# Kernel optimization log

Hardware: AMD Instinct MI355X
Metric: run time of the kernel (lower is better)

Reference implementation:

```python
import jax, jax.numpy as jnp
import numpy as np

BETA = 6.0
LOG_2PI = float(np.log(2.0 * np.pi))


def setup_inputs() -> dict:
    key = jax.random.key(0)
    k1, k2, k3, k4 = jax.random.split(key, 4)
    B, L = 2048, 64
    kl = jax.random.uniform(k1, (B, L), dtype=jnp.float32)
    z_mean = jax.random.normal(k2, (B, L), dtype=jnp.float32)
    z_logvar = jax.random.normal(k3, (B, L), dtype=jnp.float32)
    z_sampled = jax.random.normal(k4, (B, L), dtype=jnp.float32)
    return {"kl": kl, "z_mean": z_mean, "z_logvar": z_logvar, "z_sampled": z_sampled}


def gaussian_log_density(samples, mean, log_var):
    # samples: [B,1,L], mean/log_var: [1,B,L] -> [B,B,L]
    tmp = samples - mean
    return -0.5 * (tmp * tmp * jnp.exp(-log_var) + log_var + LOG_2PI)


def total_correlation(z, z_mean, z_logvar):
    # [B, B, L]: log q(z_i_l | x_j)
    log_qz_prob = gaussian_log_density(z[:, None, :], z_mean[None, :, :], z_logvar[None, :, :])
    # sum_l logsumexp_j -> [B]
    log_qz_product = jnp.sum(jax.scipy.special.logsumexp(log_qz_prob, axis=1), axis=1)
    # logsumexp_j sum_l -> [B]
    log_qz = jax.scipy.special.logsumexp(jnp.sum(log_qz_prob, axis=2), axis=1)
    return jnp.mean(log_qz - log_qz_product)


def reference(kl, z_mean, z_logvar, z_sampled):
    kl_loss = jnp.sum(kl)
    tc = (BETA - 1.0) * total_correlation(z_sampled, z_mean, z_logvar)
    return tc + kl_loss
```

## Files before the change

kernel.cpp:

```cpp
#include <hip/hip_runtime.h>
#include <math.h>


#define NB 2048
#define NL 64
#define NE (NB * NL)
#define BVAL 12.0f

__device__ __forceinline__ float wredsum(float v) {
#pragma unroll
  for (int o = 32; o; o >>= 1) v += __shfl_xor(v, o, 64);
  return v;
}
__device__ __forceinline__ float wredmax(float v) {
#pragma unroll
  for (int o = 32; o; o >>= 1) v = fmaxf(v, __shfl_xor(v, o, 64));
  return v;
}

__global__ __launch_bounds__(256) void ka_pre(const float* __restrict__ kl,
                                              const float* __restrict__ zm,
                                              const float* __restrict__ zlv,
                                              float4* __restrict__ PK2,
                                              float* __restrict__ A2T,
                                              float* __restrict__ MA2T,
                                              float* __restrict__ QC2,
                                              float* __restrict__ KLP,
                                              float* __restrict__ Sacc,
                                              int* __restrict__ CNT) {
  const float INVLN2 = 1.4426950408889634f;
  const float LOG2PI = 1.8378770664093453f;
  int tid = threadIdx.x;
  int e = blockIdx.x * 256 + tid;
  int j = e >> 6, l = e & 63;
  float lv = zlv[e], m = zm[e];
  float a2 = -0.5f * INVLN2 * __expf(-lv);
  float b2 = -0.5f * INVLN2 * (lv + LOG2PI);
  float c1 = -2.0f * a2 * m;
  float c0 = fmaf(a2 * m, m, b2);
  PK2[e] = make_float4(a2, c1, c0 - BVAL, 0.0f);
  A2T[l * NB + j] = a2;
  MA2T[l * NB + j] = c1;
  Sacc[e] = 0.0f;
  float q = wredsum(c0);
  if (l == 0) QC2[j] = q;
  float ks = wredsum(kl[e]);
  __shared__ float sk[4];
  if (l == 0) sk[tid >> 6] = ks;
  __syncthreads();
  if (tid == 0) KLP[blockIdx.x] = sk[0] + sk[1] + sk[2] + sk[3];
  if (blockIdx.x == 0 && tid == 0) *CNT = 0;
}

__global__ __launch_bounds__(256, 8) void kb_main(const float* __restrict__ zs,
                                                  const float* __restrict__ A2T,
                                                  const float* __restrict__ MA2T,
                                                  const float* __restrict__ QC2,
                                                  const float4* __restrict__ PK2,
                                                  float* __restrict__ TPM,
                                                  float* __restrict__ TPS,
                                                  float* __restrict__ Sacc) {
  int bid = blockIdx.x;
  int jc = bid & 7;
  int i0 = (bid >> 3) * 8;
  int tid = threadIdx.x;
  int w = tid >> 6, l = tid & 63;

  __shared__ float zsh[64][8];
  if (tid < 128) {
    int k = tid >> 1, r0 = (tid & 1) * 4;
#pragma unroll
    for (int r = 0; r < 4; ++r) zsh[k][r0 + r] = zs[(i0 + r0 + r) * NL + k];
  }
  __syncthreads();
  int j = jc * 256 + tid;
  float accv[8];
  float q = QC2[j];
#pragma unroll
  for (int r = 0; r < 8; ++r) accv[r] = q;
  for (int k = 0; k < 64; ++k) {
    float av = A2T[k * NB + j];
    float mv = MA2T[k * NB + j];
    const float4* z4 = (const float4*)&zsh[k][0];
    float4 za = z4[0], zb = z4[1];
    float zk[8] = {za.x, za.y, za.z, za.w, zb.x, zb.y, zb.z, zb.w};
#pragma unroll
    for (int r = 0; r < 8; ++r) {
      accv[r] = fmaf(zk[r] * zk[r], av, accv[r]);
      accv[r] = fmaf(zk[r], mv, accv[r]);
    }
  }
  __shared__ float lm[4][8], ls[4][8];
#pragma unroll
  for (int r = 0; r < 8; ++r) {
    float mx = wredmax(accv[r]);
    if (l == 0) lm[w][r] = mx;
  }
  __syncthreads();
  float Mt[8];
#pragma unroll
  for (int r = 0; r < 8; ++r)
    Mt[r] = fmaxf(fmaxf(lm[0][r], lm[1][r]), fmaxf(lm[2][r], lm[3][r]));
#pragma unroll
  for (int r = 0; r < 8; ++r) {
    float ss = wredsum(__builtin_amdgcn_exp2f(accv[r] - Mt[r]));
    if (l == 0) ls[w][r] = ss;
  }
  __syncthreads();
  if (tid == 0) {
#pragma unroll
    for (int r = 0; r < 8; ++r) {
      TPM[(i0 + r) * 8 + jc] = Mt[r];
      TPS[(i0 + r) * 8 + jc] = ls[0][r] + ls[1][r] + ls[2][r] + ls[3][r];
    }
  }

  const float4* p = PK2 + (size_t)(jc * 256 + w * 64) * NL + l;
  float zr[8];
#pragma unroll
  for (int r = 0; r < 8; ++r) zr[r] = zs[(i0 + r) * NL + l];
  float S[8];
#pragma unroll
  for (int r = 0; r < 8; ++r) S[r] = 0.0f;
#pragma unroll 4
  for (int jj = 0; jj < 64; ++jj) {
    float4 c = p[(size_t)jj * NL];
#pragma unroll
    for (int r = 0; r < 8; ++r) {
      float lp2 = fmaf(fmaf(zr[r], c.x, c.y), zr[r], c.z);
      S[r] += __builtin_amdgcn_exp2f(lp2);
    }
  }
  __shared__ float lss[4][8][64];
#pragma unroll
  for (int r = 0; r < 8; ++r) lss[w][r][l] = S[r];
  __syncthreads();
  for (int pp = tid; pp < 512; pp += 256) {
    int r = pp >> 6, ll = pp & 63;
    float Sc = lss[0][r][ll] + lss[1][r][ll] + lss[2][r][ll] + lss[3][r][ll];
    atomicAdd(&Sacc[(size_t)(i0 + r) * NL + ll], Sc);
  }
}

__global__ __launch_bounds__(256) void kc_fin(const float* __restrict__ Sacc,
                                              const float* __restrict__ TPM,
                                              const float* __restrict__ TPS,
                                              const float* __restrict__ KLP,
                                              float* __restrict__ PERB,
                                              int* __restrict__ CNT,
                                              float* __restrict__ out) {
  int tid = threadIdx.x;
  int w = tid >> 6, l = tid & 63;
  int i = blockIdx.x * 4 + w;
  float S = Sacc[(size_t)i * NL + l];
  float val = __builtin_amdgcn_logf(S);
  float lqp2 = wredsum(val) + 64.0f * BVAL;
  float tm = (l < 8) ? TPM[i * 8 + l] : -1e30f;
  float ts = (l < 8) ? TPS[i * 8 + l] : 0.0f;
  float Mt = wredmax(tm);
  float St = wredsum(ts * __builtin_amdgcn_exp2f(tm - Mt));
  float lqz2 = Mt + __builtin_amdgcn_logf(St);
  __shared__ float sblk[4];
  if (l == 0) sblk[w] = lqz2 - lqp2;
  __syncthreads();
  __shared__ int slast;
  if (tid == 0) {
    float v = sblk[0] + sblk[1] + sblk[2] + sblk[3];
    __hip_atomic_store(&PERB[blockIdx.x], v, __ATOMIC_RELEASE, __HIP_MEMORY_SCOPE_AGENT);
    int old = __hip_atomic_fetch_add(CNT, 1, __ATOMIC_ACQ_REL, __HIP_MEMORY_SCOPE_AGENT);
    slast = (old == 511) ? 1 : 0;
  }
  __syncthreads();
  if (!slast) return;
  float a = 0.0f, b = 0.0f;
  for (int x = tid; x < 512; x += 256) {
    a += KLP[x];
    b += __hip_atomic_load(&PERB[x], __ATOMIC_ACQUIRE, __HIP_MEMORY_SCOPE_AGENT);
  }
  float ra = wredsum(a), rb = wredsum(b);
  __shared__ float sa[4], sb[4];
  if (l == 0) {
    sa[w] = ra;
    sb[w] = rb;
  }
  __syncthreads();
  if (tid == 0) {
    const float LN2 = 0.6931471805599453f;
    float ka = sa[0] + sa[1] + sa[2] + sa[3];
    float kb = sb[0] + sb[1] + sb[2] + sb[3];
    out[0] = ka + 5.0f * LN2 * kb * (1.0f / (float)NB);
  }
}

extern "C" void kernel_launch(void* const* d_in, const int* in_sizes, int n_in,
                              void* d_out, int out_size, void* d_ws, size_t ws_size,
                              hipStream_t stream) {
  const float* kl = (const float*)d_in[0];
  const float* zm = (const float*)d_in[1];
  const float* zlv = (const float*)d_in[2];
  const float* zs = (const float*)d_in[3];
  float* ws = (float*)d_ws;

  float* PK2 = ws;
  float* A2T = PK2 + 4 * NE;
  float* MA2T = A2T + NE;
  float* QC2 = MA2T + NE;
  float* Sacc = QC2 + NB;
  float* TPM = Sacc + NE;
  float* TPS = TPM + NB * 8;
  float* KLP = TPS + NB * 8;
  float* PERB = KLP + 512;
  int* CNT = (int*)(PERB + 512);

  ka_pre<<<NE / 256, 256, 0, stream>>>(kl, zm, zlv, (float4*)PK2, A2T, MA2T, QC2,
                                       KLP, Sacc, CNT);
  kb_main<<<2048, 256, 0, stream>>>(zs, A2T, MA2T, QC2, (const float4*)PK2, TPM,
                                    TPS, Sacc);
  kc_fin<<<512, 256, 0, stream>>>(Sacc, TPM, TPS, KLP, PERB, CNT, (float*)d_out);
}
```

Baseline: 139.2 us.

## Split main kernel, use packed FMA and per-slice partial sums instead of atomics

```diff
diff --git a/kernel.cpp b/kernel.cpp
--- a/kernel.cpp
+++ b/kernel.cpp
@@ -6,6 +6,19 @@
 #define NL 64
 #define NE (NB * NL)
 #define BVAL 12.0f
+
+typedef float v2f __attribute__((ext_vector_type(2)));
+
+__device__ __forceinline__ v2f fma2(v2f a, v2f b, v2f c) {
+#if __has_builtin(__builtin_elementwise_fma)
+  return __builtin_elementwise_fma(a, b, c);
+#else
+  v2f r;
+  r.x = fmaf(a.x, b.x, c.x);
+  r.y = fmaf(a.y, b.y, c.y);
+  return r;
+#endif
+}
 
 __device__ __forceinline__ float wredsum(float v) {
 #pragma unroll
@@ -26,7 +39,6 @@
                                               float* __restrict__ MA2T,
                                               float* __restrict__ QC2,
                                               float* __restrict__ KLP,
-                                              float* __restrict__ Sacc,
                                               int* __restrict__ CNT) {
   const float INVLN2 = 1.4426950408889634f;
   const float LOG2PI = 1.8378770664093453f;
@@ -41,7 +53,6 @@
   PK2[e] = make_float4(a2, c1, c0 - BVAL, 0.0f);
   A2T[l * NB + j] = a2;
   MA2T[l * NB + j] = c1;
-  Sacc[e] = 0.0f;
   float q = wredsum(c0);
   if (l == 0) QC2[j] = q;
   float ks = wredsum(kl[e]);
@@ -52,20 +63,17 @@
   if (blockIdx.x == 0 && tid == 0) *CNT = 0;
 }
 
-__global__ __launch_bounds__(256, 8) void kb_main(const float* __restrict__ zs,
-                                                  const float* __restrict__ A2T,
-                                                  const float* __restrict__ MA2T,
-                                                  const float* __restrict__ QC2,
-                                                  const float4* __restrict__ PK2,
-                                                  float* __restrict__ TPM,
-                                                  float* __restrict__ TPS,
-                                                  float* __restrict__ Sacc) {
-  int bid = blockIdx.x;
-  int jc = bid & 7;
-  int i0 = (bid >> 3) * 8;
-  int tid = threadIdx.x;
-  int w = tid >> 6, l = tid & 63;
-
+__global__ __launch_bounds__(256) void k2_t(const float* __restrict__ zs,
+                                            const float* __restrict__ A2T,
+                                            const float* __restrict__ MA2T,
+                                            const float* __restrict__ QC2,
+                                            float* __restrict__ TPM,
+                                            float* __restrict__ TPS) {
+  int jc = blockIdx.x;
+  int i0 = blockIdx.y * 8;
+  int tid = threadIdx.x;
+  int w = tid >> 6;
+  int j = jc * 256 + tid;
   __shared__ float zsh[64][8];
   if (tid < 128) {
     int k = tid >> 1, r0 = (tid & 1) * 4;
@@ -73,7 +81,6 @@
     for (int r = 0; r < 4; ++r) zsh[k][r0 + r] = zs[(i0 + r0 + r) * NL + k];
   }
   __syncthreads();
-  int j = jc * 256 + tid;
   float accv[8];
   float q = QC2[j];
 #pragma unroll
@@ -94,7 +101,7 @@
 #pragma unroll
   for (int r = 0; r < 8; ++r) {
     float mx = wredmax(accv[r]);
-    if (l == 0) lm[w][r] = mx;
+    if ((tid & 63) == 0) lm[w][r] = mx;
   }
   __syncthreads();
   float Mt[8];
@@ -104,7 +111,7 @@
 #pragma unroll
   for (int r = 0; r < 8; ++r) {
     float ss = wredsum(__builtin_amdgcn_exp2f(accv[r] - Mt[r]));
-    if (l == 0) ls[w][r] = ss;
+    if ((tid & 63) == 0) ls[w][r] = ss;
   }
   __syncthreads();
   if (tid == 0) {
@@ -114,35 +121,48 @@
       TPS[(i0 + r) * 8 + jc] = ls[0][r] + ls[1][r] + ls[2][r] + ls[3][r];
     }
   }
-
-  const float4* p = PK2 + (size_t)(jc * 256 + w * 64) * NL + l;
-  float zr[8];
-#pragma unroll
-  for (int r = 0; r < 8; ++r) zr[r] = zs[(i0 + r) * NL + l];
-  float S[8];
-#pragma unroll
-  for (int r = 0; r < 8; ++r) S[r] = 0.0f;
-#pragma unroll 4
-  for (int jj = 0; jj < 64; ++jj) {
+}
+
+__global__ __launch_bounds__(256) void k3_lse(const float* __restrict__ zs,
+                                              const float4* __restrict__ PK2,
+                                              float* __restrict__ SP) {
+  int jc = blockIdx.x;
+  int i0 = blockIdx.y * 16;
+  int tid = threadIdx.x;
+  int w = tid >> 6, l = tid & 63;
+  const float4* p = PK2 + (size_t)(jc * 128 + w * 32) * NL + l;
+  v2f zr[8];
+#pragma unroll
+  for (int r = 0; r < 8; ++r) {
+    zr[r].x = zs[(i0 + 2 * r) * NL + l];
+    zr[r].y = zs[(i0 + 2 * r + 1) * NL + l];
+  }
+  v2f S[8];
+#pragma unroll
+  for (int r = 0; r < 8; ++r) S[r] = (v2f){0.0f, 0.0f};
+#pragma unroll 2
+  for (int jj = 0; jj < 32; ++jj) {
     float4 c = p[(size_t)jj * NL];
+    v2f ca = (v2f){c.x, c.x}, cb = (v2f){c.y, c.y}, cc = (v2f){c.z, c.z};
 #pragma unroll
     for (int r = 0; r < 8; ++r) {
-      float lp2 = fmaf(fmaf(zr[r], c.x, c.y), zr[r], c.z);
-      S[r] += __builtin_amdgcn_exp2f(lp2);
+      v2f t = fma2(zr[r], ca, cb);
+      v2f lp = fma2(t, zr[r], cc);
+      v2f e;
+      e.x = __builtin_amdgcn_exp2f(lp.x);
+      e.y = __builtin_amdgcn_exp2f(lp.y);
+      S[r] += e;
     }
   }
-  __shared__ float lss[4][8][64];
-#pragma unroll
-  for (int r = 0; r < 8; ++r) lss[w][r][l] = S[r];
-  __syncthreads();
-  for (int pp = tid; pp < 512; pp += 256) {
-    int r = pp >> 6, ll = pp & 63;
-    float Sc = lss[0][r][ll] + lss[1][r][ll] + lss[2][r][ll] + lss[3][r][ll];
-    atomicAdd(&Sacc[(size_t)(i0 + r) * NL + ll], Sc);
-  }
-}
-
-__global__ __launch_bounds__(256) void kc_fin(const float* __restrict__ Sacc,
+  float* sp = SP + (size_t)(jc * 4 + w) * NE;
+#pragma unroll
+  for (int r = 0; r < 8; ++r) {
+    sp[(size_t)(i0 + 2 * r) * NL + l] = S[r].x;
+    sp[(size_t)(i0 + 2 * r + 1) * NL + l] = S[r].y;
+  }
+}
+
+__global__ __launch_bounds__(256) void kc_fin(const float* __restrict__ SP,
                                               const float* __restrict__ TPM,
                                               const float* __restrict__ TPS,
                                               const float* __restrict__ KLP,
@@ -152,7 +172,9 @@
   int tid = threadIdx.x;
   int w = tid >> 6, l = tid & 63;
   int i = blockIdx.x * 4 + w;
-  float S = Sacc[(size_t)i * NL + l];
+  float S = 0.0f;
+#pragma unroll 8
+  for (int s = 0; s < 64; ++s) S += SP[(size_t)s * NE + (size_t)i * NL + l];
   float val = __builtin_amdgcn_logf(S);
   float lqp2 = wredsum(val) + 64.0f * BVAL;
   float tm = (l < 8) ? TPM[i * 8 + l] : -1e30f;
@@ -205,16 +227,16 @@
   float* A2T = PK2 + 4 * NE;
   float* MA2T = A2T + NE;
   float* QC2 = MA2T + NE;
-  float* Sacc = QC2 + NB;
-  float* TPM = Sacc + NE;
+  float* SP = QC2 + NB;
+  float* TPM = SP + 64 * (size_t)NE;
   float* TPS = TPM + NB * 8;
   float* KLP = TPS + NB * 8;
   float* PERB = KLP + 512;
   int* CNT = (int*)(PERB + 512);
 
   ka_pre<<<NE / 256, 256, 0, stream>>>(kl, zm, zlv, (float4*)PK2, A2T, MA2T, QC2,
-                                       KLP, Sacc, CNT);
-  kb_main<<<2048, 256, 0, stream>>>(zs, A2T, MA2T, QC2, (const float4*)PK2, TPM,
-                                    TPS, Sacc);
-  kc_fin<<<512, 256, 0, stream>>>(Sacc, TPM, TPS, KLP, PERB, CNT, (float*)d_out);
-}
+                                       KLP, CNT);
+  k2_t<<<dim3(8, NB / 8), 256, 0, stream>>>(zs, A2T, MA2T, QC2, TPM, TPS);
+  k3_lse<<<dim3(16, NB / 16), 256, 0, stream>>>(zs, (const float4*)PK2, SP);
+  kc_fin<<<512, 256, 0, stream>>>(SP, TPM, TPS, KLP, PERB, CNT, (float*)d_out);
+}
```

New measurement: 149.0 us. +7.1%, slower.
